# Kernel tuning notes

Measured on AMD Instinct MI355X. Metric: run time of the kernel, lower is better.

## Reference

```python
import jax, jax.numpy as jnp
import numpy as np
from jax import lax

B, C, H, W = 2, 256, 128, 128
NC, NP = 80, 9  # num_classes, num_points (3x3 dcn kernel)
PAD = 1


def conv2d(x, w, b=None, pad=1):
    out = lax.conv_general_dilated(x, w, (1, 1), [(pad, pad), (pad, pad)],
                                   dimension_numbers=('NCHW', 'OIHW', 'NCHW'))
    if b is not None:
        out = out + b[None, :, None, None]
    return out


def bilinear_sample(img_bhwc, py, px):
    # zero-padded bilinear sampling; py/px: [B,H,W] float coords
    Hi, Wi = img_bhwc.shape[1], img_bhwc.shape[2]
    y0 = jnp.floor(py)
    x0 = jnp.floor(px)
    wy1 = py - y0
    wx1 = px - x0

    def gather(yc, xc, w):
        valid = (yc >= 0) & (yc <= Hi - 1) & (xc >= 0) & (xc <= Wi - 1)
        yi = jnp.clip(yc, 0, Hi - 1).astype(jnp.int32)
        xi = jnp.clip(xc, 0, Wi - 1).astype(jnp.int32)
        v = jax.vmap(lambda im, yy, xx: im[yy, xx])(img_bhwc, yi, xi)  # [B,H,W,C]
        return v * (w * valid)[..., None]

    return (gather(y0, x0, (1 - wy1) * (1 - wx1)) + gather(y0, x0 + 1, (1 - wy1) * wx1)
            + gather(y0 + 1, x0, wy1 * (1 - wx1)) + gather(y0 + 1, x0 + 1, wy1 * wx1))


def deform_conv(x, offset, weight, mask=None, pad=1):
    # x: [B,C,H,W]; offset: [B,2K,H,W] interleaved (dy,dx) per kernel point;
    # mask: [B,K,H,W] or None (modulated DCN multiplies sampled value by mask as-is)
    kh, kw = weight.shape[2], weight.shape[3]
    xb = jnp.transpose(x, (0, 2, 3, 1))  # [B,H,W,C]
    gy, gx = jnp.meshgrid(jnp.arange(x.shape[2], dtype=x.dtype),
                          jnp.arange(x.shape[3], dtype=x.dtype), indexing='ij')
    acc = 0.
    for k in range(kh * kw):  # fixed structural loop over 9 kernel points
        ky, kx = k // kw, k % kw
        py = gy[None] + (ky - pad) + offset[:, 2 * k]
        px = gx[None] + (kx - pad) + offset[:, 2 * k + 1]
        val = bilinear_sample(xb, py, px)  # [B,H,W,C]
        if mask is not None:
            val = val * mask[:, k][..., None]
        acc = acc + jnp.einsum('bhwc,oc->bohw', val, weight[:, :, ky, kx])
    return acc


def setup_inputs() -> dict:
    key = jax.random.key(0)
    ks = jax.random.split(key, 16)
    d = {"x": jax.random.normal(ks[0], (B, C, H, W), jnp.float32)}

    def w(k, shape):
        return jax.random.normal(k, shape, jnp.float32) * 0.01

    i = 1
    for j in range(3):
        d[f"cls_w{j}"] = w(ks[i], (C, C, 3, 3)); i += 1
        d[f"cls_b{j}"] = jnp.zeros((C,), jnp.float32)
        d[f"reg_w{j}"] = w(ks[i], (C, C, 3, 3)); i += 1
        d[f"reg_b{j}"] = jnp.zeros((C,), jnp.float32)
    d["init_conv_w"] = w(ks[i], (C, C, 3, 3)); i += 1
    d["init_conv_b"] = jnp.zeros((C,), jnp.float32)
    d["init_out_w"] = w(ks[i], (3 * NP, C, 1, 1)); i += 1
    d["init_out_b"] = jnp.zeros((3 * NP,), jnp.float32)
    d["dcn_cls_w"] = w(ks[i], (C, C, 3, 3)); i += 1  # ModulatedDeformConv (bias=False)
    d["cls_out_w"] = w(ks[i], (NC, C, 1, 1)); i += 1
    d["cls_out_b"] = jnp.full((NC,), -4.59511985013459, jnp.float32)  # bias_init_with_prob(0.01)
    d["dcn_ref_w"] = w(ks[i], (C, C, 3, 3)); i += 1  # DeformConv (bias=False)
    d["ref_out_w"] = w(ks[i], (2 * NP, C, 1, 1)); i += 1
    d["ref_out_b"] = jnp.zeros((2 * NP,), jnp.float32)
    return d


def reference(x, cls_w0, cls_b0, reg_w0, reg_b0, cls_w1, cls_b1, reg_w1, reg_b1,
              cls_w2, cls_b2, reg_w2, reg_b2, init_conv_w, init_conv_b,
              init_out_w, init_out_b, dcn_cls_w, cls_out_w, cls_out_b,
              dcn_ref_w, ref_out_w, ref_out_b):
    relu = jax.nn.relu
    cls_feat = x
    for wgt, b in ((cls_w0, cls_b0), (cls_w1, cls_b1), (cls_w2, cls_b2)):
        cls_feat = relu(conv2d(cls_feat, wgt, b, 1))
    pts_feat = x
    for wgt, b in ((reg_w0, reg_b0), (reg_w1, reg_b1), (reg_w2, reg_b2)):
        pts_feat = relu(conv2d(pts_feat, wgt, b, 1))

    pts_out_init = conv2d(relu(conv2d(pts_feat, init_conv_w, init_conv_b, 1)),
                          init_out_w, init_out_b, 0)  # [B,27,H,W]
    o1, o2, mask = (pts_out_init[:, :NP], pts_out_init[:, NP:2 * NP],
                    pts_out_init[:, 2 * NP:])
    offset = jnp.concatenate([o1, o2], axis=1)  # dcn_offset (points_init = 0)

    cls_out = conv2d(relu(deform_conv(cls_feat, offset, dcn_cls_w, mask)),
                     cls_out_w, cls_out_b, 0)
    pts_out_refine = conv2d(relu(deform_conv(pts_feat, offset, dcn_ref_w)),
                            ref_out_w, ref_out_b, 0)
    pts_out_refine = pts_out_refine + lax.stop_gradient(offset)

    # pts2wh_offsets
    pts = pts_out_refine.reshape(B, NP, 2, H, W)
    pts_mean = pts.mean(axis=1, keepdims=True)          # [B,1,2,H,W]
    wh = jnp.abs(pts + pts_mean).max(axis=1)            # [B,2,H,W]
    reg = pts_mean[:, 0]                                # [B,2,H,W]
    return (cls_out, wh, reg)
```

## Files before the change

### kernel.cpp

```cpp
#include <hip/hip_runtime.h>

#define Bn 2
#define Cn 256
#define Hn 128
#define Wn 128
#define HWn 16384
#define NCn 80

typedef __attribute__((ext_vector_type(4))) float f32x4;
typedef __attribute__((ext_vector_type(8))) short bf16x8;

__device__ __forceinline__ float b2f(unsigned short h) {
    union { unsigned u; float f; } x; x.u = ((unsigned)h) << 16; return x.f;
}
__device__ __forceinline__ float blo(unsigned u) {
    union { unsigned u; float f; } x; x.u = u << 16; return x.f;
}
__device__ __forceinline__ float bhi(unsigned u) {
    union { unsigned u; float f; } x; x.u = u & 0xffff0000u; return x.f;
}
__device__ __forceinline__ unsigned short f2bf(float f) {
    union { float f; unsigned u; } x; x.f = f;
    unsigned u = x.u + 0x7fffu + ((x.u >> 16) & 1u);
    return (unsigned short)(u >> 16);
}

#define GLOAD16(gp, lp) __builtin_amdgcn_global_load_lds( \
    (__attribute__((address_space(1))) unsigned int*)(gp), \
    (__attribute__((address_space(3))) unsigned int*)(lp), 16, 0, 0)

__global__ void zeroK(unsigned short* z) { z[threadIdx.x] = 0; }

__global__ __launch_bounds__(256) void xinK(const float* __restrict__ x,
                                            unsigned short* __restrict__ o) {
    __shared__ float tb[32][33];
    const int b = blockIdx.z;
    const int hw0 = blockIdx.x * 32, c0 = blockIdx.y * 32;
    const int tx = threadIdx.x & 31, ty = threadIdx.x >> 5;
    const float* ip = x + ((size_t)(b * Cn + c0)) * HWn + hw0;
#pragma unroll
    for (int r = 0; r < 4; ++r) tb[ty + 8 * r][tx] = ip[(size_t)(ty + 8 * r) * HWn + tx];
    __syncthreads();
    unsigned short* op = o + ((size_t)(b * HWn + hw0)) * Cn + c0;
#pragma unroll
    for (int r = 0; r < 4; ++r) op[(size_t)(ty + 8 * r) * Cn + tx] = f2bf(tb[tx][ty + 8 * r]);
}

struct WPtrs { const float* p[9]; };
__global__ __launch_bounds__(256) void repackAll(WPtrs wsrc, unsigned short* __restrict__ dst) {
    const int widx = blockIdx.y;
    const int t = blockIdx.x * 256 + threadIdx.x;
    const int ic = t & 255, oc = (t >> 8) & 255, k = t >> 16;
    dst[(size_t)widx * 589824 + t] = f2bf(wsrc.p[widx][((size_t)(oc * Cn + ic)) * 9 + k]);
}

struct HPtrs { const float* w[3]; };
__global__ __launch_bounds__(256) void repackHeads(HPtrs hs, unsigned short* __restrict__ dst) {
    const int t = blockIdx.x * 256 + threadIdx.x;
    const int ic = t & 255, row = t >> 8;
    int which, oc, OC;
    if (row < 32)       { which = 0; oc = row;       OC = 27; }
    else if (row < 128) { which = 1; oc = row - 32;  OC = 80; }
    else                { which = 2; oc = row - 128; OC = 18; }
    dst[t] = (oc < OC) ? f2bf(hs.w[which][(size_t)oc * Cn + ic]) : (unsigned short)0;
}

__global__ __launch_bounds__(256, 2) void convGemm(const unsigned short* __restrict__ feat,
                                                   const unsigned short* __restrict__ Wp,
                                                   const float* __restrict__ bias,
                                                   const unsigned short* __restrict__ zb,
                                                   unsigned short* __restrict__ out) {
    __shared__ __align__(16) unsigned short lA[2][8192];
    __shared__ __align__(16) unsigned short lB[2][8192];
    const int tid = threadIdx.x;
    const int l = tid & 63, w = tid >> 6;
    const int w_oc = w & 1, w_px = w >> 1;
    const int ry = (blockIdx.x & 7) * 32 + (blockIdx.x >> 3);
    const int b = ry >> 7, y = ry & 127;
    const int oc0 = blockIdx.y * 128;
    const int lr = l & 15, lg = l >> 4;

    int rI[4], cI[4], dI[4];
#pragma unroll
    for (int i = 0; i < 4; ++i) {
        int ps = (i * 4 + w) * 64 + l;
        rI[i] = ps >> 3;
        cI[i] = ((ps & 7) ^ (rI[i] & 7)) * 8;
        dI[i] = (i * 4 + w) * 512;
    }

    f32x4 acc[4][4];
#pragma unroll
    for (int i = 0; i < 4; ++i)
#pragma unroll
        for (int j = 0; j < 4; ++j) acc[i][j] = (f32x4){0.f, 0.f, 0.f, 0.f};

    auto stage = [&](int p, int bufIdx) {
        const int k = p >> 2, c0 = (p & 3) * 64;
        const int dy = k / 3 - 1, dx = k % 3 - 1;
        const int yy = y + dy;
        const bool vy = (unsigned)yy < (unsigned)Hn;
        const size_t fbase = ((size_t)(b * Hn + yy)) * Wn;
        const unsigned short* wk = Wp + (size_t)k * 65536 + (size_t)oc0 * Cn + c0;
        unsigned short* la = lA[bufIdx];
        unsigned short* lb = lB[bufIdx];
#pragma unroll
        for (int i = 0; i < 4; ++i)
            GLOAD16(wk + rI[i] * Cn + cI[i], la + dI[i]);
#pragma unroll
        for (int i = 0; i < 4; ++i) {
            const int pxs = rI[i] + dx;
            const unsigned short* g = (vy && (unsigned)pxs < (unsigned)Wn)
                ? feat + ((fbase + pxs) * Cn + c0 + cI[i])
                : zb;
            GLOAD16(g, lb + dI[i]);
        }
    };

    stage(0, 0);
    __syncthreads();

#pragma unroll 1
    for (int p = 0; p < 36; ++p) {
        const int cur = p & 1;
        if (p < 35) stage(p + 1, cur ^ 1);
        const unsigned short* la = lA[cur];
        const unsigned short* lb = lB[cur];
#pragma unroll
        for (int h = 0; h < 2; ++h) {
            const int ch = h * 4 + lg;
            bf16x8 av[4], bv[4];
#pragma unroll
            for (int fm = 0; fm < 4; ++fm) {
                const int row = w_oc * 64 + fm * 16 + lr;
                av[fm] = *(const bf16x8*)&la[row * 64 + ((ch ^ (row & 7)) * 8)];
            }
#pragma unroll
            for (int fn = 0; fn < 4; ++fn) {
                const int row = w_px * 64 + fn * 16 + lr;
                bv[fn] = *(const bf16x8*)&lb[row * 64 + ((ch ^ (row & 7)) * 8)];
            }
#pragma unroll
            for (int fm = 0; fm < 4; ++fm)
#pragma unroll
                for (int fn = 0; fn < 4; ++fn)
                    acc[fm][fn] = __builtin_amdgcn_mfma_f32_16x16x32_bf16(
                        av[fm], bv[fn], acc[fm][fn], 0, 0, 0);
        }
        __syncthreads();
    }

#pragma unroll
    for (int fm = 0; fm < 4; ++fm) {
        const int ocb = oc0 + w_oc * 64 + fm * 16 + lg * 4;
        const float b0 = bias[ocb], b1 = bias[ocb + 1], b2 = bias[ocb + 2], b3 = bias[ocb + 3];
#pragma unroll
        for (int fn = 0; fn < 4; ++fn) {
            const int px = w_px * 64 + fn * 16 + lr;
            f32x4 v = acc[fm][fn];
            unsigned u0 = (unsigned)f2bf(fmaxf(v[0] + b0, 0.f)) | ((unsigned)f2bf(fmaxf(v[1] + b1, 0.f)) << 16);
            unsigned u1 = (unsigned)f2bf(fmaxf(v[2] + b2, 0.f)) | ((unsigned)f2bf(fmaxf(v[3] + b3, 0.f)) << 16);
            uint2 st; st.x = u0; st.y = u1;
            *(uint2*)&out[((size_t)ry * Wn + px) * Cn + ocb] = st;
        }
    }
}

template <bool HASMASK>
__global__ __launch_bounds__(512, 4) void dcnGemm(const unsigned short* __restrict__ feat,
                                                  const float* __restrict__ o27,
                                                  const unsigned short* __restrict__ Wp,
                                                  unsigned short* __restrict__ out) {
    __shared__ __align__(16) unsigned short lA[2][16384];
    __shared__ __align__(16) unsigned short lB[2][4096];
    const int tid = threadIdx.x;
    const int l = tid & 63, w = tid >> 6;
    const int w_oc = w & 3, w_px = w >> 2;
    const int g = (blockIdx.x & 7) * 64 + (blockIdx.x >> 3);
    const int ry = g >> 1, st = g & 1;
    const int b = ry >> 7, y = ry & 127;
    const int x0 = st * 64;
    const int lr = l & 15, lg = l >> 4;

    int rIA[4], cIA[4], dIA[4];
#pragma unroll
    for (int i = 0; i < 4; ++i) {
        int ps = (i * 8 + w) * 64 + l;
        rIA[i] = ps >> 3;
        cIA[i] = ((ps & 7) ^ (rIA[i] & 7)) * 8;
        dIA[i] = (i * 8 + w) * 512;
    }

    const int sp = tid >> 3;
    const int pc = tid & 7;
    const int xg = x0 + sp;

    const float* ob = o27 + (size_t)b * 27 * HWn + y * Wn + xg;
    const unsigned short* fb = feat + (size_t)b * HWn * Cn;

    f32x4 acc[4][2];
#pragma unroll
    for (int i = 0; i < 4; ++i)
#pragma unroll
        for (int j = 0; j < 2; ++j) acc[i][j] = (f32x4){0.f, 0.f, 0.f, 0.f};

    int ci0, ci1, ci2, ci3;
    float cw0, cw1, cw2, cw3;

    auto sampParams = [&](int k) {
        const float offy = ob[(size_t)(2 * k) * HWn];
        const float offx = ob[(size_t)(2 * k + 1) * HWn];
        const float m = HASMASK ? ob[(size_t)(18 + k) * HWn] : 1.f;
        const float py = (float)(y + k / 3 - 1) + offy;
        const float px = (float)(xg + k % 3 - 1) + offx;
        const float y0f = floorf(py), x0f = floorf(px);
        const float wy1 = py - y0f, wx1 = px - x0f;
        const int iy0 = (int)y0f, ix0 = (int)x0f;
        const int iy1 = iy0 + 1, ix1 = ix0 + 1;
        const bool vy0 = (unsigned)iy0 < (unsigned)Hn, vy1 = (unsigned)iy1 < (unsigned)Hn;
        const bool vx0 = (unsigned)ix0 < (unsigned)Wn, vx1 = (unsigned)ix1 < (unsigned)Wn;
        const int yc0 = min(max(iy0, 0), Hn - 1), yc1 = min(max(iy1, 0), Hn - 1);
        const int xc0 = min(max(ix0, 0), Wn - 1), xc1 = min(max(ix1, 0), Wn - 1);
        cw0 = (vy0 && vx0) ? (1.f - wy1) * (1.f - wx1) * m : 0.f;
        cw1 = (vy0 && vx1) ? (1.f - wy1) * wx1 * m : 0.f;
        cw2 = (vy1 && vx0) ? wy1 * (1.f - wx1) * m : 0.f;
        cw3 = (vy1 && vx1) ? wy1 * wx1 * m : 0.f;
        ci0 = (yc0 * Wn + xc0) * Cn;
        ci1 = (yc0 * Wn + xc1) * Cn;
        ci2 = (yc1 * Wn + xc0) * Cn;
        ci3 = (yc1 * Wn + xc1) * Cn;
    };

    auto stage = [&](int p, int bufIdx) {
        const int k = p >> 2, c0 = (p & 3) * 64;
        const unsigned short* wk = Wp + (size_t)k * 65536 + c0;
        unsigned short* la = lA[bufIdx];
#pragma unroll
        for (int i = 0; i < 4; ++i)
            GLOAD16(wk + rIA[i] * Cn + cIA[i], la + dIA[i]);
        if ((p & 3) == 0) sampParams(k);
        const int cb = c0 + pc * 8;
        int4 q0 = *(const int4*)(fb + ci0 + cb);
        int4 q1 = *(const int4*)(fb + ci1 + cb);
        int4 q2 = *(const int4*)(fb + ci2 + cb);
        int4 q3 = *(const int4*)(fb + ci3 + cb);
        unsigned u[4];
#pragma unroll
        for (int jj = 0; jj < 4; ++jj) {
            const unsigned a0 = ((const unsigned*)&q0)[jj];
            const unsigned a1 = ((const unsigned*)&q1)[jj];
            const unsigned a2 = ((const unsigned*)&q2)[jj];
            const unsigned a3 = ((const unsigned*)&q3)[jj];
            float e0 = cw0 * blo(a0) + cw1 * blo(a1) + cw2 * blo(a2) + cw3 * blo(a3);
            float e1 = cw0 * bhi(a0) + cw1 * bhi(a1) + cw2 * bhi(a2) + cw3 * bhi(a3);
            u[jj] = (unsigned)f2bf(e0) | ((unsigned)f2bf(e1) << 16);
        }
        int4 pk; pk.x = u[0]; pk.y = u[1]; pk.z = u[2]; pk.w = u[3];
        *(int4*)&lB[bufIdx][sp * 64 + ((pc ^ (sp & 7)) * 8)] = pk;
    };

    stage(0, 0);
    __syncthreads();

#pragma unroll 1
    for (int p = 0; p < 36; ++p) {
        const int cur = p & 1;
        if (p < 35) stage(p + 1, cur ^ 1);
        const unsigned short* la = lA[cur];
        const unsigned short* lb = lB[cur];
#pragma unroll
        for (int h = 0; h < 2; ++h) {
            const int ch = h * 4 + lg;
            bf16x8 av[4], bv[2];
#pragma unroll
            for (int fm = 0; fm < 4; ++fm) {
                const int row = w_oc * 64 + fm * 16 + lr;
                av[fm] = *(const bf16x8*)&la[row * 64 + ((ch ^ (row & 7)) * 8)];
            }
#pragma unroll
            for (int fn = 0; fn < 2; ++fn) {
                const int row = w_px * 32 + fn * 16 + lr;
                bv[fn] = *(const bf16x8*)&lb[row * 64 + ((ch ^ (row & 7)) * 8)];
            }
#pragma unroll
            for (int fm = 0; fm < 4; ++fm)
#pragma unroll
                for (int fn = 0; fn < 2; ++fn)
                    acc[fm][fn] = __builtin_amdgcn_mfma_f32_16x16x32_bf16(
                        av[fm], bv[fn], acc[fm][fn], 0, 0, 0);
        }
        __syncthreads();
    }

#pragma unroll
    for (int fm = 0; fm < 4; ++fm) {
        const int ocb = w_oc * 64 + fm * 16 + lg * 4;
#pragma unroll
        for (int fn = 0; fn < 2; ++fn) {
            const int px = x0 + w_px * 32 + fn * 16 + lr;
            f32x4 v = acc[fm][fn];
            unsigned u0 = (unsigned)f2bf(fmaxf(v[0], 0.f)) | ((unsigned)f2bf(fmaxf(v[1], 0.f)) << 16);
            unsigned u1 = (unsigned)f2bf(fmaxf(v[2], 0.f)) | ((unsigned)f2bf(fmaxf(v[3], 0.f)) << 16);
            uint2 stv; stv.x = u0; stv.y = u1;
            *(uint2*)&out[((size_t)ry * Wn + px) * Cn + ocb] = stv;
        }
    }
}

template <int OC, int PM, bool ADD>
__global__ __launch_bounds__(256, 2) void headGemm(const unsigned short* __restrict__ feat,
                                                   const unsigned short* __restrict__ Wp,
                                                   const float* __restrict__ bias,
                                                   float* __restrict__ out,
                                                   const float* __restrict__ add,
                                                   int addC) {
    constexpr int MF = PM / 16;
    constexpr int NA = PM * 8 / 256;
    __shared__ __align__(16) unsigned short lA[PM * 64];
    __shared__ __align__(16) unsigned short lB[128 * 64];
    const int tid = threadIdx.x;
    const int l = tid & 63, w = tid >> 6;
    const int ry = (blockIdx.x & 7) * 32 + (blockIdx.x >> 3);
    const int b = ry >> 7, y = ry & 127;
    const int lr = l & 15, lg = l >> 4;

    int rIA[NA], cIA[NA], dIA[NA];
#pragma unroll
    for (int i = 0; i < NA; ++i) {
        int ps = (i * 4 + w) * 64 + l;
        rIA[i] = ps >> 3;
        cIA[i] = ((ps & 7) ^ (rIA[i] & 7)) * 8;
        dIA[i] = (i * 4 + w) * 512;
    }
    int rIB[4], cIB[4], dIB[4];
#pragma unroll
    for (int i = 0; i < 4; ++i) {
        int ps = (i * 4 + w) * 64 + l;
        rIB[i] = ps >> 3;
        cIB[i] = ((ps & 7) ^ (rIB[i] & 7)) * 8;
        dIB[i] = (i * 4 + w) * 512;
    }

    f32x4 acc[MF][2];
#pragma unroll
    for (int i = 0; i < MF; ++i)
#pragma unroll
        for (int j = 0; j < 2; ++j) acc[i][j] = (f32x4){0.f, 0.f, 0.f, 0.f};

    const unsigned short* frow = feat + ((size_t)ry * Wn) * Cn;

#pragma unroll 1
    for (int cc = 0; cc < 4; ++cc) {
        const int c0 = cc * 64;
#pragma unroll
        for (int i = 0; i < NA; ++i)
            GLOAD16(Wp + (size_t)rIA[i] * Cn + c0 + cIA[i], &lA[dIA[i]]);
#pragma unroll
        for (int i = 0; i < 4; ++i)
            GLOAD16(frow + (size_t)rIB[i] * Cn + c0 + cIB[i], &lB[dIB[i]]);
        __syncthreads();
#pragma unroll
        for (int h = 0; h < 2; ++h) {
            const int ch = h * 4 + lg;
            bf16x8 av[MF], bv[2];
#pragma unroll
            for (int fm = 0; fm < MF; ++fm) {
                const int row = fm * 16 + lr;
                av[fm] = *(const bf16x8*)&lA[row * 64 + ((ch ^ (row & 7)) * 8)];
            }
#pragma unroll
            for (int fn = 0; fn < 2; ++fn) {
                const int row = w * 32 + fn * 16 + lr;
                bv[fn] = *(const bf16x8*)&lB[row * 64 + ((ch ^ (row & 7)) * 8)];
            }
#pragma unroll
            for (int fm = 0; fm < MF; ++fm)
#pragma unroll
                for (int fn = 0; fn < 2; ++fn)
                    acc[fm][fn] = __builtin_amdgcn_mfma_f32_16x16x32_bf16(
                        av[fm], bv[fn], acc[fm][fn], 0, 0, 0);
        }
        __syncthreads();
    }

#pragma unroll
    for (int fm = 0; fm < MF; ++fm) {
        const int ocb = fm * 16 + lg * 4;
        if (ocb >= OC) break;
#pragma unroll
        for (int j = 0; j < 4; ++j) {
            const int oc = ocb + j;
            if (oc >= OC) break;
            const float bs = bias[oc];
#pragma unroll
            for (int fn = 0; fn < 2; ++fn) {
                const int px = w * 32 + fn * 16 + lr;
                float r = acc[fm][fn][j] + bs;
                const size_t oidx = ((size_t)(b * OC + oc)) * HWn + y * Wn + px;
                if (ADD) r += add[((size_t)(b * addC + oc)) * HWn + y * Wn + px];
                out[oidx] = r;
            }
        }
    }
}

__global__ __launch_bounds__(256) void postK(const float* __restrict__ r18,
                                             float* __restrict__ wh,
                                             float* __restrict__ reg) {
    const int hw = (blockIdx.x & 63) * 256 + threadIdx.x;
    const int b = blockIdx.x >> 6;
    const float* p = r18 + (size_t)(b * 18) * HWn + hw;
    float v[18];
#pragma unroll
    for (int c = 0; c < 18; ++c) v[c] = p[(size_t)c * HWn];
    float s0 = 0.f, s1 = 0.f;
#pragma unroll
    for (int q = 0; q < 9; ++q) { s0 += v[2 * q]; s1 += v[2 * q + 1]; }
    float m0 = s0 * (1.f / 9.f), m1 = s1 * (1.f / 9.f);
    float w0 = 0.f, w1 = 0.f;
#pragma unroll
    for (int q = 0; q < 9; ++q) {
        w0 = fmaxf(w0, fabsf(v[2 * q] + m0));
        w1 = fmaxf(w1, fabsf(v[2 * q + 1] + m1));
    }
    wh[(size_t)(b * 2 + 0) * HWn + hw] = w0;
    wh[(size_t)(b * 2 + 1) * HWn + hw] = w1;
    reg[(size_t)(b * 2 + 0) * HWn + hw] = m0;
    reg[(size_t)(b * 2 + 1) * HWn + hw] = m1;
}

extern "C" void kernel_launch(void* const* d_in, const int* in_sizes, int n_in,
                              void* d_out, int out_size, void* d_ws, size_t ws_size,
                              hipStream_t stream) {
    const float* x           = (const float*)d_in[0];
    const float* cls_w0      = (const float*)d_in[1];
    const float* cls_b0      = (const float*)d_in[2];
    const float* reg_w0      = (const float*)d_in[3];
    const float* reg_b0      = (const float*)d_in[4];
    const float* cls_w1      = (const float*)d_in[5];
    const float* cls_b1      = (const float*)d_in[6];
    const float* reg_w1      = (const float*)d_in[7];
    const float* reg_b1      = (const float*)d_in[8];
    const float* cls_w2      = (const float*)d_in[9];
    const float* cls_b2      = (const float*)d_in[10];
    const float* reg_w2      = (const float*)d_in[11];
    const float* reg_b2      = (const float*)d_in[12];
    const float* init_conv_w = (const float*)d_in[13];
    const float* init_conv_b = (const float*)d_in[14];
    const float* init_out_w  = (const float*)d_in[15];
    const float* init_out_b  = (const float*)d_in[16];
    const float* dcn_cls_w   = (const float*)d_in[17];
    const float* cls_out_w   = (const float*)d_in[18];
    const float* cls_out_b   = (const float*)d_in[19];
    const float* dcn_ref_w   = (const float*)d_in[20];
    const float* ref_out_w   = (const float*)d_in[21];
    const float* ref_out_b   = (const float*)d_in[22];

    float* out = (float*)d_out;

    char* ws = (char*)d_ws;
    const size_t IMG = (size_t)Bn * HWn * Cn * sizeof(unsigned short);
    unsigned short* Xb  = (unsigned short*)ws; ws += IMG;
    unsigned short* T1  = (unsigned short*)ws; ws += IMG;
    unsigned short* T2  = (unsigned short*)ws; ws += IMG;
    unsigned short* CLS = (unsigned short*)ws; ws += IMG;
    unsigned short* PTS = (unsigned short*)ws; ws += IMG;
    float* O27 = (float*)ws; ws += (size_t)Bn * 27 * HWn * sizeof(float);
    float* R18 = (float*)ws; ws += (size_t)Bn * 18 * HWn * sizeof(float);
    const size_t WSZ = (size_t)9 * Cn * Cn;
    unsigned short* Wpk = (unsigned short*)ws; ws += 9 * WSZ * sizeof(unsigned short);
    unsigned short* WhAll = (unsigned short*)ws; ws += 160 * Cn * sizeof(unsigned short);
    unsigned short* ZB = (unsigned short*)ws;  ws += 512;

    unsigned short* W_cls0 = Wpk + 0 * WSZ;
    unsigned short* W_cls1 = Wpk + 1 * WSZ;
    unsigned short* W_cls2 = Wpk + 2 * WSZ;
    unsigned short* W_reg0 = Wpk + 3 * WSZ;
    unsigned short* W_reg1 = Wpk + 4 * WSZ;
    unsigned short* W_reg2 = Wpk + 5 * WSZ;
    unsigned short* W_init = Wpk + 6 * WSZ;
    unsigned short* W_dcls = Wpk + 7 * WSZ;
    unsigned short* W_dref = Wpk + 8 * WSZ;
    unsigned short* Wh27 = WhAll;
    unsigned short* Wh80 = WhAll + 32 * Cn;
    unsigned short* Wh18 = WhAll + 128 * Cn;

    const dim3 blk(256);
    const dim3 cgrd(256, 2);
    const dim3 xgrd(512, 8, Bn);

    zeroK<<<1, 128, 0, stream>>>(ZB);
    WPtrs wp;
    wp.p[0] = cls_w0; wp.p[1] = cls_w1; wp.p[2] = cls_w2;
    wp.p[3] = reg_w0; wp.p[4] = reg_w1; wp.p[5] = reg_w2;
    wp.p[6] = init_conv_w; wp.p[7] = dcn_cls_w; wp.p[8] = dcn_ref_w;
    repackAll<<<dim3(2304, 9), blk, 0, stream>>>(wp, Wpk);
    HPtrs hp; hp.w[0] = init_out_w; hp.w[1] = cls_out_w; hp.w[2] = ref_out_w;
    repackHeads<<<160, blk, 0, stream>>>(hp, WhAll);
    xinK<<<xgrd, blk, 0, stream>>>(x, Xb);

    convGemm<<<cgrd, blk, 0, stream>>>(Xb, W_cls0, cls_b0, ZB, T1);
    convGemm<<<cgrd, blk, 0, stream>>>(T1, W_cls1, cls_b1, ZB, T2);
    convGemm<<<cgrd, blk, 0, stream>>>(T2, W_cls2, cls_b2, ZB, CLS);
    convGemm<<<cgrd, blk, 0, stream>>>(Xb, W_reg0, reg_b0, ZB, T1);
    convGemm<<<cgrd, blk, 0, stream>>>(T1, W_reg1, reg_b1, ZB, T2);
    convGemm<<<cgrd, blk, 0, stream>>>(T2, W_reg2, reg_b2, ZB, PTS);
    convGemm<<<cgrd, blk, 0, stream>>>(PTS, W_init, init_conv_b, ZB, T1);
    headGemm<27, 32, false><<<256, blk, 0, stream>>>(T1, Wh27, init_out_b, O27, nullptr, 0);
    dcnGemm<true><<<512, dim3(512), 0, stream>>>(CLS, O27, W_dcls, T2);
    headGemm<80, 96, false><<<256, blk, 0, stream>>>(T2, Wh80, cls_out_b, out, nullptr, 0);
    dcnGemm<false><<<512, dim3(512), 0, stream>>>(PTS, O27, W_dref, T1);
    headGemm<18, 32, true><<<256, blk, 0, stream>>>(T1, Wh18, ref_out_b, R18, O27, 27);

    postK<<<128, blk, 0, stream>>>(R18,
                                   out + (size_t)Bn * NCn * HWn,
                                   out + (size_t)Bn * NCn * HWn + (size_t)Bn * 2 * HWn);
}
```

Before: 611.4 us.

## Batch cls/reg conv chains, pipeline DCN corner loads, fuse postprocess into head

The independent cls and reg conv towers now run as paired jobs in a single launch via blockIdx.z, doubling the grid per launch and cutting the number of launches. In the DCN GEMM, the gather loads for the next stage are issued before the MFMA loop and the interpolation and LDS write happen after it, so the global latency can overlap with compute. The points post-processing (mean and wh) is fused into the final head GEMM epilogue through shared memory, which removes the postK kernel and the R18 buffer. The weight repack now reads nine contiguous floats per thread instead of doing strided loads. The trade-offs are higher register pressure in dcnGemm and extra buffer aliasing to keep track of.

```diff
diff --git a/kernel.cpp b/kernel.cpp
--- a/kernel.cpp
+++ b/kernel.cpp
@@ -10,9 +10,6 @@
 typedef __attribute__((ext_vector_type(4))) float f32x4;
 typedef __attribute__((ext_vector_type(8))) short bf16x8;
 
-__device__ __forceinline__ float b2f(unsigned short h) {
-    union { unsigned u; float f; } x; x.u = ((unsigned)h) << 16; return x.f;
-}
 __device__ __forceinline__ float blo(unsigned u) {
     union { unsigned u; float f; } x; x.u = u << 16; return x.f;
 }
@@ -48,10 +45,16 @@
 
 struct WPtrs { const float* p[9]; };
 __global__ __launch_bounds__(256) void repackAll(WPtrs wsrc, unsigned short* __restrict__ dst) {
-    const int widx = blockIdx.y;
     const int t = blockIdx.x * 256 + threadIdx.x;
-    const int ic = t & 255, oc = (t >> 8) & 255, k = t >> 16;
-    dst[(size_t)widx * 589824 + t] = f2bf(wsrc.p[widx][((size_t)(oc * Cn + ic)) * 9 + k]);
+    const int widx = t >> 16;
+    const int r = t & 65535;
+    const float* s = wsrc.p[widx] + (size_t)r * 9;
+    float v[9];
+#pragma unroll
+    for (int k = 0; k < 9; ++k) v[k] = s[k];
+    unsigned short* d = dst + (size_t)widx * 589824 + r;
+#pragma unroll
+    for (int k = 0; k < 9; ++k) d[(size_t)k * 65536] = f2bf(v[k]);
 }
 
 struct HPtrs { const float* w[3]; };
@@ -65,11 +68,20 @@
     dst[t] = (oc < OC) ? f2bf(hs.w[which][(size_t)oc * Cn + ic]) : (unsigned short)0;
 }
 
-__global__ __launch_bounds__(256, 2) void convGemm(const unsigned short* __restrict__ feat,
-                                                   const unsigned short* __restrict__ Wp,
-                                                   const float* __restrict__ bias,
-                                                   const unsigned short* __restrict__ zb,
-                                                   unsigned short* __restrict__ out) {
+struct CJobs {
+    const unsigned short* feat[2];
+    const unsigned short* W[2];
+    const float* bias[2];
+    unsigned short* out[2];
+};
+__global__ __launch_bounds__(256, 2) void convGemm(CJobs jobs,
+                                                   const unsigned short* __restrict__ zb) {
+    const int jz = blockIdx.z;
+    const unsigned short* feat = jobs.feat[jz];
+    const unsigned short* Wp = jobs.W[jz];
+    const float* bias = jobs.bias[jz];
+    unsigned short* outp = jobs.out[jz];
+
     __shared__ __align__(16) unsigned short lA[2][8192];
     __shared__ __align__(16) unsigned short lB[2][8192];
     const int tid = threadIdx.x;
@@ -161,7 +173,7 @@
             unsigned u0 = (unsigned)f2bf(fmaxf(v[0] + b0, 0.f)) | ((unsigned)f2bf(fmaxf(v[1] + b1, 0.f)) << 16);
             unsigned u1 = (unsigned)f2bf(fmaxf(v[2] + b2, 0.f)) | ((unsigned)f2bf(fmaxf(v[3] + b3, 0.f)) << 16);
             uint2 st; st.x = u0; st.y = u1;
-            *(uint2*)&out[((size_t)ry * Wn + px) * Cn + ocb] = st;
+            *(uint2*)&outp[((size_t)ry * Wn + px) * Cn + ocb] = st;
         }
     }
 }
@@ -194,6 +206,7 @@
     const int sp = tid >> 3;
     const int pc = tid & 7;
     const int xg = x0 + sp;
+    const int wslot = sp * 64 + ((pc ^ (sp & 7)) * 8);
 
     const float* ob = o27 + (size_t)b * 27 * HWn + y * Wn + xg;
     const unsigned short* fb = feat + (size_t)b * HWn * Cn;
@@ -231,19 +244,23 @@
         ci3 = (yc1 * Wn + xc1) * Cn;
     };
 
-    auto stage = [&](int p, int bufIdx) {
+    int4 q0, q1, q2, q3;
+    auto cornerLoads = [&](int p) {
+        const int cb = (p & 3) * 64 + pc * 8;
+        q0 = *(const int4*)(fb + ci0 + cb);
+        q1 = *(const int4*)(fb + ci1 + cb);
+        q2 = *(const int4*)(fb + ci2 + cb);
+        q3 = *(const int4*)(fb + ci3 + cb);
+    };
+    auto stageA = [&](int p, int bufIdx) {
         const int k = p >> 2, c0 = (p & 3) * 64;
         const unsigned short* wk = Wp + (size_t)k * 65536 + c0;
         unsigned short* la = lA[bufIdx];
 #pragma unroll
         for (int i = 0; i < 4; ++i)
             GLOAD16(wk + rIA[i] * Cn + cIA[i], la + dIA[i]);
-        if ((p & 3) == 0) sampParams(k);
-        const int cb = c0 + pc * 8;
-        int4 q0 = *(const int4*)(fb + ci0 + cb);
-        int4 q1 = *(const int4*)(fb + ci1 + cb);
-        int4 q2 = *(const int4*)(fb + ci2 + cb);
-        int4 q3 = *(const int4*)(fb + ci3 + cb);
+    };
+    auto interpWrite = [&](int bufIdx) {
         unsigned u[4];
 #pragma unroll
         for (int jj = 0; jj < 4; ++jj) {
@@ -256,16 +273,23 @@
             u[jj] = (unsigned)f2bf(e0) | ((unsigned)f2bf(e1) << 16);
         }
         int4 pk; pk.x = u[0]; pk.y = u[1]; pk.z = u[2]; pk.w = u[3];
-        *(int4*)&lB[bufIdx][sp * 64 + ((pc ^ (sp & 7)) * 8)] = pk;
+        *(int4*)&lB[bufIdx][wslot] = pk;
     };
 
-    stage(0, 0);
+    sampParams(0);
+    stageA(0, 0);
+    cornerLoads(0);
+    interpWrite(0);
     __syncthreads();
 
 #pragma unroll 1
     for (int p = 0; p < 36; ++p) {
         const int cur = p & 1;
-        if (p < 35) stage(p + 1, cur ^ 1);
+        if (p < 35) {
+            if (((p + 1) & 3) == 0) sampParams((p + 1) >> 2);
+            stageA(p + 1, cur ^ 1);
+            cornerLoads(p + 1);
+        }
         const unsigned short* la = lA[cur];
         const unsigned short* lb = lB[cur];
 #pragma unroll
@@ -289,6 +313,7 @@
                     acc[fm][fn] = __builtin_amdgcn_mfma_f32_16x16x32_bf16(
                         av[fm], bv[fn], acc[fm][fn], 0, 0, 0);
         }
+        if (p < 35) interpWrite(cur ^ 1);
         __syncthreads();
     }
 
@@ -307,17 +332,19 @@
     }
 }
 
-template <int OC, int PM, bool ADD>
+template <int OC, int PM, bool ADD, bool POST>
 __global__ __launch_bounds__(256, 2) void headGemm(const unsigned short* __restrict__ feat,
                                                    const unsigned short* __restrict__ Wp,
                                                    const float* __restrict__ bias,
                                                    float* __restrict__ out,
                                                    const float* __restrict__ add,
-                                                   int addC) {
+                                                   int addC,
+                                                   float* __restrict__ reg) {
     constexpr int MF = PM / 16;
     constexpr int NA = PM * 8 / 256;
     __shared__ __align__(16) unsigned short lA[PM * 64];
     __shared__ __align__(16) unsigned short lB[128 * 64];
+    __shared__ float lR[POST ? 18 : 1][POST ? 128 : 1];
     const int tid = threadIdx.x;
     const int l = tid & 63, w = tid >> 6;
     const int ry = (blockIdx.x & 7) * 32 + (blockIdx.x >> 3);
@@ -383,50 +410,67 @@
         __syncthreads();
     }
 
-#pragma unroll
-    for (int fm = 0; fm < MF; ++fm) {
-        const int ocb = fm * 16 + lg * 4;
-        if (ocb >= OC) break;
-#pragma unroll
-        for (int j = 0; j < 4; ++j) {
-            const int oc = ocb + j;
-            if (oc >= OC) break;
-            const float bs = bias[oc];
-#pragma unroll
-            for (int fn = 0; fn < 2; ++fn) {
-                const int px = w * 32 + fn * 16 + lr;
-                float r = acc[fm][fn][j] + bs;
-                const size_t oidx = ((size_t)(b * OC + oc)) * HWn + y * Wn + px;
-                if (ADD) r += add[((size_t)(b * addC + oc)) * HWn + y * Wn + px];
-                out[oidx] = r;
-            }
-        }
-    }
-}
-
-__global__ __launch_bounds__(256) void postK(const float* __restrict__ r18,
-                                             float* __restrict__ wh,
-                                             float* __restrict__ reg) {
-    const int hw = (blockIdx.x & 63) * 256 + threadIdx.x;
-    const int b = blockIdx.x >> 6;
-    const float* p = r18 + (size_t)(b * 18) * HWn + hw;
-    float v[18];
-#pragma unroll
-    for (int c = 0; c < 18; ++c) v[c] = p[(size_t)c * HWn];
-    float s0 = 0.f, s1 = 0.f;
-#pragma unroll
-    for (int q = 0; q < 9; ++q) { s0 += v[2 * q]; s1 += v[2 * q + 1]; }
-    float m0 = s0 * (1.f / 9.f), m1 = s1 * (1.f / 9.f);
-    float w0 = 0.f, w1 = 0.f;
-#pragma unroll
-    for (int q = 0; q < 9; ++q) {
-        w0 = fmaxf(w0, fabsf(v[2 * q] + m0));
-        w1 = fmaxf(w1, fabsf(v[2 * q + 1] + m1));
-    }
-    wh[(size_t)(b * 2 + 0) * HWn + hw] = w0;
-    wh[(size_t)(b * 2 + 1) * HWn + hw] = w1;
-    reg[(size_t)(b * 2 + 0) * HWn + hw] = m0;
-    reg[(size_t)(b * 2 + 1) * HWn + hw] = m1;
+    if (!POST) {
+#pragma unroll
+        for (int fm = 0; fm < MF; ++fm) {
+            const int ocb = fm * 16 + lg * 4;
+            if (ocb >= OC) break;
+#pragma unroll
+            for (int j = 0; j < 4; ++j) {
+                const int oc = ocb + j;
+                if (oc >= OC) break;
+                const float bs = bias[oc];
+#pragma unroll
+                for (int fn = 0; fn < 2; ++fn) {
+                    const int px = w * 32 + fn * 16 + lr;
+                    float r = acc[fm][fn][j] + bs;
+                    if (ADD) r += add[((size_t)(b * addC + oc)) * HWn + y * Wn + px];
+                    out[((size_t)(b * OC + oc)) * HWn + y * Wn + px] = r;
+                }
+            }
+        }
+    } else {
+#pragma unroll
+        for (int fm = 0; fm < MF; ++fm) {
+            const int ocb = fm * 16 + lg * 4;
+#pragma unroll
+            for (int j = 0; j < 4; ++j) {
+                const int oc = ocb + j;
+                if (oc < 18) {
+                    const float bs = bias[oc];
+#pragma unroll
+                    for (int fn = 0; fn < 2; ++fn) {
+                        const int px = w * 32 + fn * 16 + lr;
+                        float r = acc[fm][fn][j] + bs
+                                + add[((size_t)(b * addC + oc)) * HWn + y * Wn + px];
+                        lR[oc][px] = r;
+                    }
+                }
+            }
+        }
+        __syncthreads();
+        if (tid < 128) {
+            const int px = tid;
+            float v[18];
+#pragma unroll
+            for (int c = 0; c < 18; ++c) v[c] = lR[c][px];
+            float s0 = 0.f, s1 = 0.f;
+#pragma unroll
+            for (int q = 0; q < 9; ++q) { s0 += v[2 * q]; s1 += v[2 * q + 1]; }
+            float m0 = s0 * (1.f / 9.f), m1 = s1 * (1.f / 9.f);
+            float w0 = 0.f, w1 = 0.f;
+#pragma unroll
+            for (int q = 0; q < 9; ++q) {
+                w0 = fmaxf(w0, fabsf(v[2 * q] + m0));
+                w1 = fmaxf(w1, fabsf(v[2 * q + 1] + m1));
+            }
+            const size_t hw = (size_t)y * Wn + px;
+            out[(size_t)(b * 2 + 0) * HWn + hw] = w0;
+            out[(size_t)(b * 2 + 1) * HWn + hw] = w1;
+            reg[(size_t)(b * 2 + 0) * HWn + hw] = m0;
+            reg[(size_t)(b * 2 + 1) * HWn + hw] = m1;
+        }
+    }
 }
 
 extern "C" void kernel_launch(void* const* d_in, const int* in_sizes, int n_in,
@@ -460,13 +504,11 @@
 
     char* ws = (char*)d_ws;
     const size_t IMG = (size_t)Bn * HWn * Cn * sizeof(unsigned short);
-    unsigned short* Xb  = (unsigned short*)ws; ws += IMG;
-    unsigned short* T1  = (unsigned short*)ws; ws += IMG;
-    unsigned short* T2  = (unsigned short*)ws; ws += IMG;
-    unsigned short* CLS = (unsigned short*)ws; ws += IMG;
-    unsigned short* PTS = (unsigned short*)ws; ws += IMG;
+    unsigned short* B0 = (unsigned short*)ws; ws += IMG;
+    unsigned short* B1 = (unsigned short*)ws; ws += IMG;
+    unsigned short* B2 = (unsigned short*)ws; ws += IMG;
+    unsigned short* B3 = (unsigned short*)ws; ws += IMG;
     float* O27 = (float*)ws; ws += (size_t)Bn * 27 * HWn * sizeof(float);
-    float* R18 = (float*)ws; ws += (size_t)Bn * 18 * HWn * sizeof(float);
     const size_t WSZ = (size_t)9 * Cn * Cn;
     unsigned short* Wpk = (unsigned short*)ws; ws += 9 * WSZ * sizeof(unsigned short);
     unsigned short* WhAll = (unsigned short*)ws; ws += 160 * Cn * sizeof(unsigned short);
@@ -486,7 +528,6 @@
     unsigned short* Wh18 = WhAll + 128 * Cn;
 
     const dim3 blk(256);
-    const dim3 cgrd(256, 2);
     const dim3 xgrd(512, 8, Bn);
 
     zeroK<<<1, 128, 0, stream>>>(ZB);
@@ -494,25 +535,31 @@
     wp.p[0] = cls_w0; wp.p[1] = cls_w1; wp.p[2] = cls_w2;
     wp.p[3] = reg_w0; wp.p[4] = reg_w1; wp.p[5] = reg_w2;
     wp.p[6] = init_conv_w; wp.p[7] = dcn_cls_w; wp.p[8] = dcn_ref_w;
-    repackAll<<<dim3(2304, 9), blk, 0, stream>>>(wp, Wpk);
+    repackAll<<<2304, blk, 0, stream>>>(wp, Wpk);
     HPtrs hp; hp.w[0] = init_out_w; hp.w[1] = cls_out_w; hp.w[2] = ref_out_w;
     repackHeads<<<160, blk, 0, stream>>>(hp, WhAll);
-    xinK<<<xgrd, blk, 0, stream>>>(x, Xb);
-
-    convGemm<<<cgrd, blk, 0, stream>>>(Xb, W_cls0, cls_b0, ZB, T1);
-    convGemm<<<cgrd, blk, 0, stream>>>(T1, W_cls1, cls_b1, ZB, T2);
-    convGemm<<<cgrd, blk, 0, stream>>>(T2, W_cls2, cls_b2, ZB, CLS);
-    convGemm<<<cgrd, blk, 0, stream>>>(Xb, W_reg0, reg_b0, ZB, T1);
-    convGemm<<<cgrd, blk, 0, stream>>>(T1, W_reg1, reg_b1, ZB, T2);
-    convGemm<<<cgrd, blk, 0, stream>>>(T2, W_reg2, reg_b2, ZB, PTS);
-    convGemm<<<cgrd, blk, 0, stream>>>(PTS, W_init, init_conv_b, ZB, T1);
-    headGemm<27, 32, false><<<256, blk, 0, stream>>>(T1, Wh27, init_out_b, O27, nullptr, 0);
-    dcnGemm<true><<<512, dim3(512), 0, stream>>>(CLS, O27, W_dcls, T2);
-    headGemm<80, 96, false><<<256, blk, 0, stream>>>(T2, Wh80, cls_out_b, out, nullptr, 0);
-    dcnGemm<false><<<512, dim3(512), 0, stream>>>(PTS, O27, W_dref, T1);
-    headGemm<18, 32, true><<<256, blk, 0, stream>>>(T1, Wh18, ref_out_b, R18, O27, 27);
-
-    postK<<<128, blk, 0, stream>>>(R18,
-                                   out + (size_t)Bn * NCn * HWn,
-                                   out + (size_t)Bn * NCn * HWn + (size_t)Bn * 2 * HWn);
-}
+    xinK<<<xgrd, blk, 0, stream>>>(x, B0);
+
+    CJobs j;
+    j.feat[0] = B0; j.W[0] = W_cls0; j.bias[0] = cls_b0; j.out[0] = B1;
+    j.feat[1] = B0; j.W[1] = W_reg0; j.bias[1] = reg_b0; j.out[1] = B2;
+    convGemm<<<dim3(256, 2, 2), blk, 0, stream>>>(j, ZB);
+    j.feat[0] = B1; j.W[0] = W_cls1; j.bias[0] = cls_b1; j.out[0] = B3;
+    j.feat[1] = B2; j.W[1] = W_reg1; j.bias[1] = reg_b1; j.out[1] = B0;
+    convGemm<<<dim3(256, 2, 2), blk, 0, stream>>>(j, ZB);
+    j.feat[0] = B3; j.W[0] = W_cls2; j.bias[0] = cls_b2; j.out[0] = B1;
+    j.feat[1] = B0; j.W[1] = W_reg2; j.bias[1] = reg_b2; j.out[1] = B2;
+    convGemm<<<dim3(256, 2, 2), blk, 0, stream>>>(j, ZB);
+    j.feat[0] = B2; j.W[0] = W_init; j.bias[0] = init_conv_b; j.out[0] = B3;
+    j.feat[1] = B2; j.W[1] = W_init; j.bias[1] = init_conv_b; j.out[1] = B3;
+    convGemm<<<dim3(256, 2, 1), blk, 0, stream>>>(j, ZB);
+    headGemm<27, 32, false, false><<<256, blk, 0, stream>>>(B3, Wh27, init_out_b, O27, nullptr, 0, nullptr);
+    dcnGemm<true><<<512, dim3(512), 0, stream>>>(B1, O27, W_dcls, B0);
+    headGemm<80, 96, false, false><<<256, blk, 0, stream>>>(B0, Wh80, cls_out_b, out, nullptr, 0, nullptr);
+    dcnGemm<false><<<512, dim3(512), 0, stream>>>(B2, O27, W_dref, B3);
+    headGemm<18, 32, true, true><<<256, blk, 0, stream>>>(
+        B3, Wh18, ref_out_b,
+        out + (size_t)Bn * NCn * HWn,
+        O27, 27,
+        out + (size_t)Bn * NCn * HWn + (size_t)Bn * 2 * HWn);
+}
```

Result: faster. 584.3 us (-4.4%).
